# Kernel optimization log

Hardware: AMD Instinct MI355X
Metric: run time of the kernel (lower is better)

Reference implementation:

```python
import math
import jax, jax.numpy as jnp
import numpy as np

B, N, C = 2, 2048, 1024
H = 16
D = C // H  # 64
LN_EPS = 1e-5


def setup_inputs() -> dict:
    key = jax.random.key(0)
    ks = jax.random.split(key, 5)
    x = jax.random.normal(ks[0], (B, N, C), dtype=jnp.float32)
    w_qkv = jax.random.normal(ks[1], (C, 3 * C), dtype=jnp.float32) * 0.02
    w_proj = jax.random.normal(ks[2], (C, C), dtype=jnp.float32) * 0.02
    b_proj = jnp.zeros((C,), dtype=jnp.float32)
    ln_w = jnp.ones((D,), dtype=jnp.float32) + jax.random.normal(ks[3], (D,), dtype=jnp.float32) * 0.02
    ln_b = jax.random.normal(ks[4], (D,), dtype=jnp.float32) * 0.02
    return {"x": x, "w_qkv": w_qkv, "w_proj": w_proj, "b_proj": b_proj,
            "ln_w": ln_w, "ln_b": ln_b}


def _layernorm(t, w, b):
    mu = jnp.mean(t, axis=-1, keepdims=True)
    var = jnp.var(t, axis=-1, keepdims=True)
    return (t - mu) * jax.lax.rsqrt(var + LN_EPS) * w + b


def reference(x, w_qkv, w_proj, b_proj, ln_w, ln_b):
    b, n, c = x.shape
    h, d = H, c // H
    # QKV projection (no bias): [b,n,3c] -> [3,b,h,n,d]
    qkv = (x @ w_qkv).reshape(b, n, 3, h, d).transpose(2, 0, 3, 1, 4)
    q, k, v = qkv[0], qkv[1], qkv[2]
    # per-head LayerNorm on q and k (qk_norm)
    q = _layernorm(q, ln_w, ln_b)
    k = _layernorm(k, ln_w, ln_b)
    # NOTE: source multiplies q by sqrt(head_dim) (faithful to original)
    q = q * jnp.asarray(math.sqrt(d), dtype=q.dtype)
    scores = jnp.einsum('bhnd,bhmd->bhnm', q, k)  # [b,h,n,n]
    mask_value = -jnp.finfo(scores.dtype).max
    causal = jnp.tril(jnp.ones((n, n), dtype=bool))
    scores = jnp.where(causal, scores, mask_value)
    attn = jax.nn.softmax(scores, axis=-1)
    out = jnp.einsum('bhnm,bhmd->bhnd', attn, v)  # [b,h,n,d]
    out = out.transpose(0, 2, 1, 3).reshape(b, n, c)  # b n (h d)
    return out @ w_proj + b_proj
```

## Files before the change

kernel.cpp:

```cpp
#include <hip/hip_runtime.h>

#define LOG2E 1.4426950408889634f

typedef _Float16 f16x8_t __attribute__((ext_vector_type(8)));
typedef _Float16 f16x4_t __attribute__((ext_vector_type(4)));
typedef float    f32x4_t __attribute__((ext_vector_type(4)));

#define MFMA32(a, b, c) __builtin_amdgcn_mfma_f32_16x16x32_f16(a, b, c, 0, 0, 0)
#define MFMA16(a, b, c) __builtin_amdgcn_mfma_f32_16x16x16f16(a, b, c, 0, 0, 0)

__device__ __forceinline__ void async_copy16(void* lds, const void* g) {
    __builtin_amdgcn_global_load_lds(
        (const __attribute__((address_space(1))) unsigned char*)g,
        (__attribute__((address_space(3))) unsigned char*)lds, 16, 0, 0);
}

__global__ void cast_f32_f16_k(const float* __restrict__ in, _Float16* __restrict__ out, int n4) {
    int i = blockIdx.x * blockDim.x + threadIdx.x;
    if (i >= n4) return;
    float4 v = ((const float4*)in)[i];
    f16x4_t o = { (_Float16)v.x, (_Float16)v.y, (_Float16)v.z, (_Float16)v.w };
    ((f16x4_t*)out)[i] = o;
}

__global__ void transpose_cast_k(const float* __restrict__ in, _Float16* __restrict__ out,
                                 int R, int C) {
    __shared__ _Float16 tl[64][65];
    const int t = threadIdx.x;
    const int c = t & 63;
    const int r4 = t >> 6;
    const int r0 = blockIdx.y * 64, c0 = blockIdx.x * 64;
#pragma unroll
    for (int i = 0; i < 16; ++i) {
        int r = r4 + i * 4;
        tl[c][r] = (_Float16)in[(size_t)(r0 + r) * C + c0 + c];
    }
    __syncthreads();
#pragma unroll
    for (int i = 0; i < 16; ++i) {
        int rr = r4 + i * 4;
        out[(size_t)(c0 + rr) * R + r0 + c] = tl[rr][c];
    }
}

__global__ void vtrans_k(const _Float16* __restrict__ qkv, _Float16* __restrict__ VTg) {
    __shared__ _Float16 tl[64][65];
    const int t = threadIdx.x;
    const int bh = blockIdx.x;
    const int b = bh >> 4, h = bh & 15;
    const int n0 = blockIdx.y * 64;
    const int c = t & 63;
    const int r4 = t >> 6;
#pragma unroll
    for (int i = 0; i < 16; ++i) {
        int r = r4 + i * 4;
        tl[c][r] = qkv[(size_t)(b * 2048 + n0 + r) * 3072 + 2048 + h * 64 + c];
    }
    __syncthreads();
#pragma unroll
    for (int i = 0; i < 16; ++i) {
        int d = r4 + i * 4;
        VTg[(size_t)bh * 131072 + (size_t)d * 2048 + n0 + c] = tl[d][c];
    }
}

template <typename OutT, bool BIAS>
__global__ __launch_bounds__(256, 2)
void gemm_f16_k(const _Float16* __restrict__ A, const _Float16* __restrict__ BT,
                OutT* __restrict__ C, const float* __restrict__ bias,
                int M, int N, int K) {
    __shared__ _Float16 As[2][128][32];
    __shared__ _Float16 Bs[2][128][32];
    const int tid = threadIdx.x;
    const int wid = tid >> 6, lane = tid & 63;
    const int qd = lane >> 4, ln = lane & 15;
    const int m0 = blockIdx.x * 128, n0 = blockIdx.y * 128;
    const int wm = (wid >> 1) * 64, wn = (wid & 1) * 64;

    f32x4_t acc[4][4] = {};

    const int srow = lane >> 2;
    const int skk  = (lane & 3) * 8;

    for (int k0 = 0; k0 < K; k0 += 64) {
        __syncthreads();
#pragma unroll
        for (int p = 0; p < 4; ++p) {
            const int seg = p * 4 + wid;
            const int s   = seg >> 3;
            const int rg  = seg & 7;
            const int row = rg * 16 + srow;
            const size_t goff = (size_t)row * K + k0 + s * 32 + skk;
            async_copy16(&As[0][0][0] + seg * 512, A  + (size_t)m0 * K + goff);
            async_copy16(&Bs[0][0][0] + seg * 512, BT + (size_t)n0 * K + goff);
        }
        __syncthreads();
#pragma unroll
        for (int s = 0; s < 2; ++s) {
            f16x8_t a[4], b[4];
#pragma unroll
            for (int i = 0; i < 4; ++i)
                a[i] = *(const f16x8_t*)&As[s][wm + i * 16 + ln][qd * 8];
#pragma unroll
            for (int j = 0; j < 4; ++j)
                b[j] = *(const f16x8_t*)&Bs[s][wn + j * 16 + ln][qd * 8];
#pragma unroll
            for (int i = 0; i < 4; ++i)
#pragma unroll
                for (int j = 0; j < 4; ++j)
                    acc[i][j] = MFMA32(a[i], b[j], acc[i][j]);
        }
    }
#pragma unroll
    for (int i = 0; i < 4; ++i)
#pragma unroll
        for (int j = 0; j < 4; ++j) {
            const int col = n0 + wn + j * 16 + ln;
            const float bv = BIAS ? bias[col] : 0.0f;
#pragma unroll
            for (int r = 0; r < 4; ++r) {
                const int row = m0 + wm + i * 16 + qd * 4 + r;
                C[(size_t)row * N + col] = (OutT)(acc[i][j][r] + bv);
            }
        }
}

__global__ __launch_bounds__(256, 2)
void gemm_f16_m64_k(const _Float16* __restrict__ A, const _Float16* __restrict__ BT,
                    float* __restrict__ C, const float* __restrict__ bias,
                    int M, int N, int K) {
    __shared__ _Float16 As[2][64][32];
    __shared__ _Float16 Bs[2][128][32];
    const int tid = threadIdx.x;
    const int wid = tid >> 6, lane = tid & 63;
    const int qd = lane >> 4, ln = lane & 15;
    const int m0 = blockIdx.x * 64, n0 = blockIdx.y * 128;
    const int wn = wid * 32;

    f32x4_t acc[4][2] = {};
    const int srow = lane >> 2;
    const int skk  = (lane & 3) * 8;

    for (int k0 = 0; k0 < K; k0 += 64) {
        __syncthreads();
#pragma unroll
        for (int p = 0; p < 2; ++p) {
            const int seg = p * 4 + wid;
            const int hidx = seg * 512 + lane * 8;
            const int s_ = hidx >> 11;
            const int row = (hidx >> 5) & 63;
            const int kk = hidx & 31;
            async_copy16(&As[0][0][0] + seg * 512,
                         A + (size_t)(m0 + row) * K + k0 + s_ * 32 + kk);
        }
#pragma unroll
        for (int p = 0; p < 4; ++p) {
            const int seg = p * 4 + wid;
            const int s   = seg >> 3;
            const int rg  = seg & 7;
            const int row = rg * 16 + srow;
            async_copy16(&Bs[0][0][0] + seg * 512,
                         BT + (size_t)(n0 + row) * K + k0 + s * 32 + skk);
        }
        __syncthreads();
#pragma unroll
        for (int s = 0; s < 2; ++s) {
            f16x8_t a[4], b[2];
#pragma unroll
            for (int i = 0; i < 4; ++i)
                a[i] = *(const f16x8_t*)&As[s][i * 16 + ln][qd * 8];
#pragma unroll
            for (int j = 0; j < 2; ++j)
                b[j] = *(const f16x8_t*)&Bs[s][wn + j * 16 + ln][qd * 8];
#pragma unroll
            for (int i = 0; i < 4; ++i)
#pragma unroll
                for (int j = 0; j < 2; ++j)
                    acc[i][j] = MFMA32(a[i], b[j], acc[i][j]);
        }
    }
#pragma unroll
    for (int i = 0; i < 4; ++i)
#pragma unroll
        for (int j = 0; j < 2; ++j) {
            const int col = n0 + wn + j * 16 + ln;
            const float bv = bias[col];
#pragma unroll
            for (int r = 0; r < 4; ++r) {
                const int row = m0 + i * 16 + qd * 4 + r;
                C[(size_t)row * N + col] = acc[i][j][r] + bv;
            }
        }
}

__global__ void ln_qk_k(const _Float16* __restrict__ qkv, const float* __restrict__ ln_w,
                        const float* __restrict__ ln_b, _Float16* __restrict__ Qb,
                        _Float16* __restrict__ Kb) {
    const int tid = threadIdx.x;
    const int wid = tid >> 6, lane = tid & 63;
    const int row = blockIdx.x * 4 + wid;
    const int t = row >> 4;
    const int h = row & 15;
    const int b = t >> 11, n = t & 2047;
    const size_t base = (size_t)t * 3072 + h * 64 + lane;
    float q = (float)qkv[base];
    float k = (float)qkv[base + 1024];
    const float wv = ln_w[lane], bv = ln_b[lane];

    float sq = q, sk = k;
#pragma unroll
    for (int m = 1; m < 64; m <<= 1) { sq += __shfl_xor(sq, m); sk += __shfl_xor(sk, m); }
    sq *= (1.0f / 64.0f); sk *= (1.0f / 64.0f);
    const float dq = q - sq, dk = k - sk;
    float vq = dq * dq, vk = dk * dk;
#pragma unroll
    for (int m = 1; m < 64; m <<= 1) { vq += __shfl_xor(vq, m); vk += __shfl_xor(vk, m); }
    vq *= (1.0f / 64.0f); vk *= (1.0f / 64.0f);
    const float yq = dq * rsqrtf(vq + 1e-5f) * wv + bv;
    const float yk = dk * rsqrtf(vk + 1e-5f) * wv + bv;
    const size_t obase = ((size_t)((b * 16 + h) * 2048 + n)) * 64 + lane;
    Qb[obase] = (_Float16)(yq * (8.0f * LOG2E));
    Kb[obase] = (_Float16)yk;
}

__global__ __launch_bounds__(256, 3)
void attn_part_k(const _Float16* __restrict__ Q, const _Float16* __restrict__ K,
                 const _Float16* __restrict__ VTg, _Float16* __restrict__ O,
                 float* __restrict__ Op, float* __restrict__ ml) {
    __shared__ _Float16 Ks[2][2][64][32];
    __shared__ _Float16 VT[2][64][64];

    const int tid = threadIdx.x;
    const int wid = tid >> 6, lane = tid & 63;
    const int qd = lane >> 4, ln = lane & 15;
    const int bh = blockIdx.x;
    const int b = bh >> 4, h = bh & 15;
    const int y = blockIdx.y;
    int band, chunk, nst;
    if (y < 16)      { band = 16 + y; chunk = 0; nst = 16; }
    else if (y < 32) { band = 47 - y; chunk = 1; nst = band - 15; }
    else             { band = 47 - y; chunk = 0; nst = band + 1; }
    const size_t kvbase = (size_t)bh * 2048 * 64;
    const size_t vtbase = (size_t)bh * 131072;
    const int qrow0 = band * 64 + wid * 16;
    const int kvbeg = chunk * 1024;

    f16x8_t qf[2];
#pragma unroll
    for (int s = 0; s < 2; ++s)
        qf[s] = *(const f16x8_t*)&Q[kvbase + (size_t)(qrow0 + ln) * 64 + s * 32 + qd * 8];

    f32x4_t o[4] = {};
    float m = -3.0e38f, l = 0.0f;

    const int vrow = lane >> 3;
    const int vY   = (lane & 7) ^ (vrow & 7);
    const int khidx_base = lane * 8;

    auto stage = [&](int buf, int kv0) {
#pragma unroll
        for (int p = 0; p < 2; ++p) {
            const int seg = p * 4 + wid;
            const int hidx = seg * 512 + khidx_base;
            const int s_ = hidx >> 11;
            const int rrow = (hidx >> 5) & 63;
            const int kk = hidx & 31;
            async_copy16(&Ks[buf][0][0][0] + seg * 512,
                         K + kvbase + (size_t)(kv0 + rrow) * 64 + s_ * 32 + kk);
        }
#pragma unroll
        for (int p = 0; p < 2; ++p) {
            const int seg = p * 4 + wid;
            const int d = seg * 8 + vrow;
            async_copy16(&VT[buf][0][0] + seg * 512,
                         VTg + vtbase + (size_t)d * 2048 + kv0 + vY * 8);
        }
    };

    stage(0, kvbeg);

    for (int st = 0; st < nst; ++st) {
        const int kv0 = kvbeg + st * 64;
        __syncthreads();
        if (st + 1 < nst) stage((st + 1) & 1, kv0 + 64);
        const int buf = st & 1;

        f16x8_t kb[4][2];
#pragma unroll
        for (int jt = 0; jt < 4; ++jt)
#pragma unroll
            for (int s = 0; s < 2; ++s)
                kb[jt][s] = *(const f16x8_t*)&Ks[buf][s][jt * 16 + ln][qd * 8];
        f16x4_t vf[4][4];
#pragma unroll
        for (int dt = 0; dt < 4; ++dt)
#pragma unroll
            for (int c = 0; c < 4; ++c)
                vf[dt][c] = *(const f16x4_t*)
                    &VT[buf][dt * 16 + ln][(((2 * c + (qd >> 1)) ^ (ln & 7)) << 3) + (qd & 1) * 4];

        f32x4_t sc[4];
#pragma unroll
        for (int jt = 0; jt < 4; ++jt) {
            f32x4_t s = {};
            s = MFMA32(kb[jt][0], qf[0], s);
            s = MFMA32(kb[jt][1], qf[1], s);
            sc[jt] = s;
        }
        if (chunk * 16 + st == band) {
            const int qq = qrow0 + ln;
#pragma unroll
            for (int c = 0; c < 4; ++c)
#pragma unroll
                for (int r = 0; r < 4; ++r)
                    if (kv0 + c * 16 + qd * 4 + r > qq) sc[c][r] = -3.0e38f;
        }
        float mx = sc[0][0];
#pragma unroll
        for (int c = 0; c < 4; ++c)
#pragma unroll
            for (int r = 0; r < 4; ++r) mx = fmaxf(mx, sc[c][r]);
        mx = fmaxf(mx, __shfl_xor(mx, 16));
        mx = fmaxf(mx, __shfl_xor(mx, 32));
        const float mn = fmaxf(m, mx);
        const float al = exp2f(m - mn);
        m = mn;
        float rs = 0.0f;
        f16x4_t pf[4];
#pragma unroll
        for (int c = 0; c < 4; ++c)
#pragma unroll
            for (int r = 0; r < 4; ++r) {
                const float p = exp2f(sc[c][r] - mn);
                rs += p;
                pf[c][r] = (_Float16)p;
            }
        l = l * al + rs;
#pragma unroll
        for (int dt = 0; dt < 4; ++dt) o[dt] *= al;
#pragma unroll
        for (int dt = 0; dt < 4; ++dt)
#pragma unroll
            for (int c = 0; c < 4; ++c)
                o[dt] = MFMA16(vf[dt][c], pf[c], o[dt]);
    }

    float lt = l + __shfl_xor(l, 16);
    lt = lt + __shfl_xor(lt, 32);

    if (band < 16) {
        const float inv = 1.0f / lt;
        const size_t base = ((size_t)(b * 2048 + qrow0 + ln)) * 1024 + h * 64 + qd * 4;
#pragma unroll
        for (int dt = 0; dt < 4; ++dt) {
            f16x4_t ov;
#pragma unroll
            for (int r = 0; r < 4; ++r) ov[r] = (_Float16)(o[dt][r] * inv);
            *(f16x4_t*)&O[base + dt * 16] = ov;
        }
    } else {
        const size_t pb = (((size_t)bh * 16 + (band - 16)) * 2 + chunk);
        const int row = wid * 16 + ln;
        float* op = Op + pb * 4096 + (size_t)row * 64 + qd * 4;
#pragma unroll
        for (int dt = 0; dt < 4; ++dt)
            *(f32x4_t*)&op[dt * 16] = o[dt];
        if (qd == 0) {
            ml[pb * 128 + row * 2]     = m;
            ml[pb * 128 + row * 2 + 1] = lt;
        }
    }
}

__global__ __launch_bounds__(256)
void attn_merge_k(const float* __restrict__ Op, const float* __restrict__ ml,
                  _Float16* __restrict__ O) {
    const int bh = blockIdx.x, bnd = blockIdx.y;
    const int b = bh >> 4, h = bh & 15;
    const int band = 16 + bnd;
    const size_t pb = ((size_t)bh * 16 + bnd) * 2;
    const int tid = threadIdx.x;
    const int row = tid >> 2;
    const int c4 = (tid & 3) * 16;
    const float m0 = ml[pb * 128 + row * 2],     l0 = ml[pb * 128 + row * 2 + 1];
    const float m1 = ml[pb * 128 + 128 + row * 2], l1 = ml[pb * 128 + 128 + row * 2 + 1];
    const float mm = fmaxf(m0, m1);
    const float a0 = exp2f(m0 - mm), a1 = exp2f(m1 - mm);
    const float inv = 1.0f / (l0 * a0 + l1 * a1);
    const float* p0 = Op + pb * 4096 + (size_t)row * 64 + c4;
    const float* p1 = p0 + 4096;
    _Float16* op = O + ((size_t)(b * 2048 + band * 64 + row)) * 1024 + h * 64 + c4;
#pragma unroll
    for (int g = 0; g < 4; ++g) {
        f32x4_t v0 = *(const f32x4_t*)&p0[g * 4];
        f32x4_t v1 = *(const f32x4_t*)&p1[g * 4];
        f16x4_t ov;
#pragma unroll
        for (int r = 0; r < 4; ++r)
            ov[r] = (_Float16)((v0[r] * a0 + v1[r] * a1) * inv);
        *(f16x4_t*)&op[g * 4] = ov;
    }
}

extern "C" void kernel_launch(void* const* d_in, const int* in_sizes, int n_in,
                              void* d_out, int out_size, void* d_ws, size_t ws_size,
                              hipStream_t stream) {
    const float* x      = (const float*)d_in[0];
    const float* w_qkv  = (const float*)d_in[1];
    const float* w_proj = (const float*)d_in[2];
    const float* b_proj = (const float*)d_in[3];
    const float* ln_w   = (const float*)d_in[4];
    const float* ln_b   = (const float*)d_in[5];
    float* out = (float*)d_out;

    char* w = (char*)d_ws;
    _Float16*  qkv    = (_Float16*)w;  w += (size_t)4096 * 3072 * 2;
    _Float16*  xh     = (_Float16*)w;  w += (size_t)4096 * 1024 * 2;
    _Float16*  wqkvT  = (_Float16*)w;  w += (size_t)3072 * 1024 * 2;
    _Float16*  wprojT = (_Float16*)w;  w += (size_t)1024 * 1024 * 2;
    _Float16*  Qb     = (_Float16*)w;  w += (size_t)32 * 2048 * 64 * 2;
    _Float16*  Kb     = (_Float16*)w;  w += (size_t)32 * 2048 * 64 * 2;
    _Float16*  VTg    = (_Float16*)w;  w += (size_t)32 * 64 * 2048 * 2;
    _Float16*  Ah     = (_Float16*)w;  w += (size_t)4096 * 1024 * 2;
    float*     Op     = (float*)w;     w += (size_t)32 * 16 * 2 * 4096 * 4;
    float*     mlb    = (float*)w;     w += (size_t)32 * 16 * 2 * 128 * 4;

    cast_f32_f16_k<<<4096, 256, 0, stream>>>(x, xh, 4096 * 1024 / 4);
    transpose_cast_k<<<dim3(48, 16), 256, 0, stream>>>(w_qkv, wqkvT, 1024, 3072);
    transpose_cast_k<<<dim3(16, 16), 256, 0, stream>>>(w_proj, wprojT, 1024, 1024);
    gemm_f16_k<_Float16, false><<<dim3(32, 24), 256, 0, stream>>>(xh, wqkvT, qkv, nullptr, 4096, 3072, 1024);
    vtrans_k<<<dim3(32, 32), 256, 0, stream>>>(qkv, VTg);
    ln_qk_k<<<16384, 256, 0, stream>>>(qkv, ln_w, ln_b, Qb, Kb);
    attn_part_k<<<dim3(32, 48), 256, 0, stream>>>(Qb, Kb, VTg, Ah, Op, mlb);
    attn_merge_k<<<dim3(32, 16), 256, 0, stream>>>(Op, mlb, Ah);
    gemm_f16_m64_k<<<dim3(64, 8), 256, 0, stream>>>(Ah, wprojT, out, b_proj, 4096, 1024, 1024);
}
```

Measured before the change: 210.0 us.

## Pre-swizzle V transpose tiles, use 16-byte LDS V reads, packed f16 conversion

The V-transpose kernel now writes each 64x64 V^T tile contiguously in global memory, already in the XOR-swizzled order the attention kernel expects. The attention stage can therefore issue linear async copies and read V fragments with 16-byte LDS loads instead of 8-byte ones. Softmax probabilities are converted with packed round-toward-zero f16 conversions, and the causal-mask test is changed to an explicit position comparison. The GEMM launch bound is also raised to three blocks per SM, which may force register spills.

```diff
diff --git a/kernel.cpp b/kernel.cpp
--- a/kernel.cpp
+++ b/kernel.cpp
@@ -4,6 +4,7 @@
 
 typedef _Float16 f16x8_t __attribute__((ext_vector_type(8)));
 typedef _Float16 f16x4_t __attribute__((ext_vector_type(4)));
+typedef _Float16 f16x2_t __attribute__((ext_vector_type(2)));
 typedef float    f32x4_t __attribute__((ext_vector_type(4)));
 
 #define MFMA32(a, b, c) __builtin_amdgcn_mfma_f32_16x16x32_f16(a, b, c, 0, 0, 0)
@@ -44,28 +45,35 @@
 }
 
 __global__ void vtrans_k(const _Float16* __restrict__ qkv, _Float16* __restrict__ VTg) {
-    __shared__ _Float16 tl[64][65];
-    const int t = threadIdx.x;
+    __shared__ _Float16 tl[64][68];
+    const int tid = threadIdx.x;
     const int bh = blockIdx.x;
     const int b = bh >> 4, h = bh & 15;
-    const int n0 = blockIdx.y * 64;
-    const int c = t & 63;
-    const int r4 = t >> 6;
+    const int t = blockIdx.y;
+    const int c = tid & 63;
+    const int r4 = tid >> 6;
 #pragma unroll
     for (int i = 0; i < 16; ++i) {
         int r = r4 + i * 4;
-        tl[c][r] = qkv[(size_t)(b * 2048 + n0 + r) * 3072 + 2048 + h * 64 + c];
+        tl[c][r] = qkv[(size_t)(b * 2048 + t * 64 + r) * 3072 + 2048 + h * 64 + c];
     }
     __syncthreads();
-#pragma unroll
-    for (int i = 0; i < 16; ++i) {
-        int d = r4 + i * 4;
-        VTg[(size_t)bh * 131072 + (size_t)d * 2048 + n0 + c] = tl[d][c];
+    const size_t obase = (size_t)bh * 131072 + (size_t)t * 4096;
+#pragma unroll
+    for (int e = 0; e < 2; ++e) {
+        const int ci = tid * 2 + e;
+        const int d = ci >> 3, w = ci & 7;
+        const int pq = w ^ (d & 7);
+        const int base = (pq >> 2) * 32 + (pq & 3) * 4;
+        f16x4_t v0 = *(const f16x4_t*)&tl[d][base];
+        f16x4_t v1 = *(const f16x4_t*)&tl[d][base + 16];
+        f16x8_t val = __builtin_shufflevector(v0, v1, 0, 1, 2, 3, 4, 5, 6, 7);
+        *(f16x8_t*)&VTg[obase + ci * 8] = val;
     }
 }
 
 template <typename OutT, bool BIAS>
-__global__ __launch_bounds__(256, 2)
+__global__ __launch_bounds__(256, 3)
 void gemm_f16_k(const _Float16* __restrict__ A, const _Float16* __restrict__ BT,
                 OutT* __restrict__ C, const float* __restrict__ bias,
                 int M, int N, int K) {
@@ -253,15 +261,11 @@
     f32x4_t o[4] = {};
     float m = -3.0e38f, l = 0.0f;
 
-    const int vrow = lane >> 3;
-    const int vY   = (lane & 7) ^ (vrow & 7);
-    const int khidx_base = lane * 8;
-
     auto stage = [&](int buf, int kv0) {
 #pragma unroll
         for (int p = 0; p < 2; ++p) {
             const int seg = p * 4 + wid;
-            const int hidx = seg * 512 + khidx_base;
+            const int hidx = seg * 512 + lane * 8;
             const int s_ = hidx >> 11;
             const int rrow = (hidx >> 5) & 63;
             const int kk = hidx & 31;
@@ -271,9 +275,8 @@
 #pragma unroll
         for (int p = 0; p < 2; ++p) {
             const int seg = p * 4 + wid;
-            const int d = seg * 8 + vrow;
             async_copy16(&VT[buf][0][0] + seg * 512,
-                         VTg + vtbase + (size_t)d * 2048 + kv0 + vY * 8);
+                         VTg + vtbase + (size_t)kv0 * 64 + seg * 512 + lane * 8);
         }
     };
 
@@ -291,13 +294,14 @@
 #pragma unroll
             for (int s = 0; s < 2; ++s)
                 kb[jt][s] = *(const f16x8_t*)&Ks[buf][s][jt * 16 + ln][qd * 8];
-        f16x4_t vf[4][4];
+        f16x8_t vf8[4][2];
 #pragma unroll
         for (int dt = 0; dt < 4; ++dt)
 #pragma unroll
-            for (int c = 0; c < 4; ++c)
-                vf[dt][c] = *(const f16x4_t*)
-                    &VT[buf][dt * 16 + ln][(((2 * c + (qd >> 1)) ^ (ln & 7)) << 3) + (qd & 1) * 4];
+            for (int pp = 0; pp < 2; ++pp) {
+                const int w = (pp * 4 + qd) ^ (ln & 7);
+                vf8[dt][pp] = *(const f16x8_t*)&VT[buf][dt * 16 + ln][w * 8];
+            }
 
         f32x4_t sc[4];
 #pragma unroll
@@ -307,7 +311,7 @@
             s = MFMA32(kb[jt][1], qf[1], s);
             sc[jt] = s;
         }
-        if (chunk * 16 + st == band) {
+        if (kv0 + 63 > qrow0) {
             const int qq = qrow0 + ln;
 #pragma unroll
             for (int c = 0; c < 4; ++c)
@@ -328,21 +332,28 @@
         float rs = 0.0f;
         f16x4_t pf[4];
 #pragma unroll
-        for (int c = 0; c < 4; ++c)
-#pragma unroll
-            for (int r = 0; r < 4; ++r) {
-                const float p = exp2f(sc[c][r] - mn);
-                rs += p;
-                pf[c][r] = (_Float16)p;
+        for (int c = 0; c < 4; ++c) {
+            float p0 = exp2f(sc[c][0] - mn);
+            float p1 = exp2f(sc[c][1] - mn);
+            float p2 = exp2f(sc[c][2] - mn);
+            float p3 = exp2f(sc[c][3] - mn);
+            rs += (p0 + p1) + (p2 + p3);
+            f16x2_t a = __builtin_bit_cast(f16x2_t, __builtin_amdgcn_cvt_pkrtz(p0, p1));
+            f16x2_t bb = __builtin_bit_cast(f16x2_t, __builtin_amdgcn_cvt_pkrtz(p2, p3));
+            pf[c] = __builtin_shufflevector(a, bb, 0, 1, 2, 3);
+        }
+        l = l * al + rs;
+#pragma unroll
+        for (int dt = 0; dt < 4; ++dt) o[dt] *= al;
+#pragma unroll
+        for (int dt = 0; dt < 4; ++dt)
+#pragma unroll
+            for (int pp = 0; pp < 2; ++pp) {
+                f16x4_t lo = __builtin_shufflevector(vf8[dt][pp], vf8[dt][pp], 0, 1, 2, 3);
+                f16x4_t hi = __builtin_shufflevector(vf8[dt][pp], vf8[dt][pp], 4, 5, 6, 7);
+                o[dt] = MFMA16(lo, pf[pp * 2 + 0], o[dt]);
+                o[dt] = MFMA16(hi, pf[pp * 2 + 1], o[dt]);
             }
-        l = l * al + rs;
-#pragma unroll
-        for (int dt = 0; dt < 4; ++dt) o[dt] *= al;
-#pragma unroll
-        for (int dt = 0; dt < 4; ++dt)
-#pragma unroll
-            for (int c = 0; c < 4; ++c)
-                o[dt] = MFMA16(vf[dt][c], pf[c], o[dt]);
     }
 
     float lt = l + __shfl_xor(l, 16);
```

Result: no change. 207.6 us (-1.1%).
